# Performance work log

Measured on AMD Instinct MI355X. Metric: run time of the kernel, lower is better.

The kernel has to match this reference:

```python
import jax, jax.numpy as jnp
import numpy as np

NUM_HEADS = 8


def _mha(x, w_in, b_in, w_out, b_out, nh=NUM_HEADS):
    # x: [B, L, H]; torch nn.MultiheadAttention (batch_first) self-attention
    B, L, H = x.shape
    dh = H // nh
    qkv = x @ w_in.T + b_in                      # [B, L, 3H]
    q, k, v = jnp.split(qkv, 3, axis=-1)
    def heads(t):
        return t.reshape(B, L, nh, dh).transpose(0, 2, 1, 3)  # [B, nh, L, dh]
    q, k, v = heads(q), heads(k), heads(v)
    scale = 1.0 / np.sqrt(dh)
    scores = jnp.einsum('bhqd,bhkd->bhqk', q * scale, k)      # [B, nh, L, L]
    attn = jax.nn.softmax(scores, axis=-1)
    out = jnp.einsum('bhqk,bhkd->bhqd', attn, v)               # [B, nh, L, dh]
    out = out.transpose(0, 2, 1, 3).reshape(B, L, H)
    return out @ w_out.T + b_out


def setup_inputs() -> dict:
    key = jax.random.key(0)
    ks = jax.random.split(key, 10)
    S, M, B, H = 64, 4, 128, 1024
    std = 0.02
    inp = {
        'hidden_states_combined': jax.random.normal(ks[0], (S, M, B, 1, H), jnp.float32),
        'mf_in_w': jax.random.normal(ks[1], (3 * H, H), jnp.float32) * std,
        'mf_in_b': jnp.zeros((3 * H,), jnp.float32),
        'mf_out_w': jax.random.normal(ks[2], (H, H), jnp.float32) * std,
        'mf_out_b': jnp.zeros((H,), jnp.float32),
        'sf_in_w': jax.random.normal(ks[3], (3 * H, H), jnp.float32) * std,
        'sf_in_b': jnp.zeros((3 * H,), jnp.float32),
        'sf_out_w': jax.random.normal(ks[4], (H, H), jnp.float32) * std,
        'sf_out_b': jnp.zeros((H,), jnp.float32),
        'pos_enc': jax.random.normal(ks[5], (1, S, H), jnp.float32) * std,
    }
    return inp


def reference(hidden_states_combined, mf_in_w, mf_in_b, mf_out_w, mf_out_b,
              sf_in_w, sf_in_b, sf_out_w, sf_out_b, pos_enc):
    S, M, B, _, H = hidden_states_combined.shape
    # [S, M, B, 1, H] -> [S, B, M, H] -> batch all steps together: [S*B, M, H]
    x = hidden_states_combined[:, :, :, 0, :].transpose(0, 2, 1, 3).reshape(S * B, M, H)
    fused = _mha(x, mf_in_w, mf_in_b, mf_out_w, mf_out_b)        # [S*B, M, H]
    fused = fused.mean(axis=1).reshape(S, B, H)                  # mean over models
    seq = fused.transpose(1, 0, 2) + pos_enc[:, :S, :]            # [B, S, H]
    enhanced = _mha(seq, sf_in_w, sf_in_b, sf_out_w, sf_out_b)   # [B, S, H]
    return enhanced.transpose(1, 0, 2)[:, :, None, :]             # [S, B, 1, H]
```

## Files before the change

kernel.cpp:

```cpp
#include <hip/hip_runtime.h>

typedef unsigned short u16;
typedef __attribute__((ext_vector_type(8))) short bf16x8;
typedef __attribute__((ext_vector_type(4))) float f32x4;

__device__ __forceinline__ u16 f2bf(float f) {
  unsigned u = __float_as_uint(f);
  u += 0x7FFFu + ((u >> 16) & 1u);
  return (u16)(u >> 16);
}
__device__ __forceinline__ float bf2f(u16 h) {
  return __uint_as_float(((unsigned)h) << 16);
}

#define GLOAD16(g, l) __builtin_amdgcn_global_load_lds( \
    (const __attribute__((address_space(1))) void*)(g), \
    (__attribute__((address_space(3))) void*)(l), 16, 0, 0)

__global__ __launch_bounds__(256) void cvtw_kernel(const float* __restrict__ in,
                                                   u16* __restrict__ out, int n4) {
  int i = blockIdx.x * 256 + threadIdx.x;
  if (i >= n4) return;
  float4 f = ((const float4*)in)[i];
  ushort4 u;
  u.x = f2bf(f.x); u.y = f2bf(f.y); u.z = f2bf(f.z); u.w = f2bf(f.w);
  ((ushort4*)out)[i] = u;
}

__global__ __launch_bounds__(256) void xcvt_kernel(const float* __restrict__ hidden,
                                                   u16* __restrict__ xb, int s0) {
  int idx = blockIdx.x * 256 + threadIdx.x;
  int h4 = idx & 255;
  int lrow = idx >> 8;
  int m = lrow & 3;
  int b = (lrow >> 2) & 127;
  int sl = lrow >> 9;
  int s = s0 + sl;
  const float4 f = *(const float4*)(hidden + (((size_t)(s * 4 + m) * 128 + b) * 1024) + h4 * 4);
  ushort4 u;
  u.x = f2bf(f.x); u.y = f2bf(f.y); u.z = f2bf(f.z); u.w = f2bf(f.w);
  *(ushort4*)(xb + (size_t)lrow * 1024 + h4 * 4) = u;
}

template <int KK>
__global__ __launch_bounds__(512, 2) void gemm8p(const u16* __restrict__ A,
                                                 const u16* __restrict__ Bw,
                                                 const float* __restrict__ bias,
                                                 u16* __restrict__ C, int N) {
  __shared__ u16 Sh[65536];
  const int t = threadIdx.x, w = t >> 6, l = t & 63;
  const int lr = l & 15, lg = l >> 4;
  const int wm = w >> 2, wn = w & 3;

  const int gx = gridDim.x;
  const int nb = gx * gridDim.y;
  const int id = blockIdx.y * gx + blockIdx.x;
  const int id2 = (id & 7) * (nb >> 3) + (id >> 3);
  const int rowBase = (id2 / gx) * 256, colBase = (id2 % gx) * 256;

  const int sslot8 = ((t & 3) ^ ((t >> 3) & 3)) * 8;
  const u16* Ag = A + (size_t)(rowBase + (t >> 2)) * KK + sslot8;
  const u16* Bg = Bw + (size_t)(colBase + (t >> 2)) * KK + sslot8;
  const size_t K128 = (size_t)128 * KK;
  const int ldsW = w * 512;

  const int fslot8 = (lg ^ ((lr >> 1) & 3)) * 8;
  const int aRowOff = (wm * 128 + lr) * 32 + fslot8;
  const int bRowOff = (wn * 64 + lr) * 32 + fslot8;

  f32x4 acc[8][4];
#pragma unroll
  for (int i = 0; i < 8; i++)
#pragma unroll
    for (int j = 0; j < 4; j++) acc[i][j] = (f32x4){0.f, 0.f, 0.f, 0.f};
  bf16x8 af[4], bfr[4];

#define STGA(tt, KH, DB) { \
    const u16* g_ = Ag + (size_t)(tt) * 64 + (KH) * 32; \
    GLOAD16(g_, Sh + ((DB) * 2 + (KH)) * 8192 + ldsW); \
    GLOAD16(g_ + K128, Sh + ((DB) * 2 + (KH)) * 8192 + 4096 + ldsW); }
#define STGB(tt, KH, DB) { \
    const u16* g_ = Bg + (size_t)(tt) * 64 + (KH) * 32; \
    GLOAD16(g_, Sh + 32768 + ((DB) * 2 + (KH)) * 8192 + ldsW); \
    GLOAD16(g_ + K128, Sh + 32768 + ((DB) * 2 + (KH)) * 8192 + 4096 + ldsW); }

#define PHASE(DD, KH, MG, DOB, STG, WT) do { \
    const u16* sa_ = Sh + ((DD) * 2 + (KH)) * 8192 + aRowOff; \
    _Pragma("unroll") \
    for (int mi = 0; mi < 4; mi++) af[mi] = *(const bf16x8*)(sa_ + ((MG) * 4 + mi) * 512); \
    if (DOB) { \
      const u16* sb_ = Sh + 32768 + ((DD) * 2 + (KH)) * 8192 + bRowOff; \
      _Pragma("unroll") \
      for (int n = 0; n < 4; n++) bfr[n] = *(const bf16x8*)(sb_ + n * 512); \
    } \
    STG; \
    __builtin_amdgcn_s_barrier(); \
    asm volatile("s_waitcnt lgkmcnt(0)" ::: "memory"); \
    __builtin_amdgcn_sched_barrier(0); \
    __builtin_amdgcn_s_setprio(1); \
    _Pragma("unroll") \
    for (int mi = 0; mi < 4; mi++) { \
      _Pragma("unroll") \
      for (int n = 0; n < 4; n++) \
        acc[(MG) * 4 + mi][n] = \
            __builtin_amdgcn_mfma_f32_16x16x32_bf16(af[mi], bfr[n], acc[(MG) * 4 + mi][n], 0, 0, 0); \
    } \
    __builtin_amdgcn_s_setprio(0); \
    WT; \
    __builtin_amdgcn_s_barrier(); \
  } while (0)

#define WTC(NN) asm volatile("s_waitcnt vmcnt(" #NN ")" ::: "memory")

  STGA(0, 0, 0); STGB(0, 0, 0);
  STGA(0, 1, 0); STGB(0, 1, 0);
  STGA(1, 0, 1); STGB(1, 0, 1);
  WTC(8);
  __builtin_amdgcn_s_barrier();

  const int NIT = KK / 128;
  int t0 = 0;
  for (int it = 0; it < NIT - 1; ++it, t0 += 2) {
    PHASE(0, 0, 0, 1, STGA(t0 + 1, 1, 1), );
    PHASE(0, 0, 1, 0, STGB(t0 + 1, 1, 1), WTC(8));
    PHASE(0, 1, 0, 1, STGA(t0 + 2, 0, 0), );
    PHASE(0, 1, 1, 0, STGB(t0 + 2, 0, 0), WTC(8));
    PHASE(1, 0, 0, 1, STGA(t0 + 2, 1, 0), );
    PHASE(1, 0, 1, 0, STGB(t0 + 2, 1, 0), WTC(8));
    PHASE(1, 1, 0, 1, STGA(t0 + 3, 0, 1), );
    PHASE(1, 1, 1, 0, STGB(t0 + 3, 0, 1), WTC(8));
  }
  PHASE(0, 0, 0, 1, STGA(t0 + 1, 1, 1), );
  PHASE(0, 0, 1, 0, STGB(t0 + 1, 1, 1), WTC(8));
  PHASE(0, 1, 0, 1, , );
  PHASE(0, 1, 1, 0, , WTC(4));
  PHASE(1, 0, 0, 1, , );
  PHASE(1, 0, 1, 0, , WTC(0));
  PHASE(1, 1, 0, 1, , );
  PHASE(1, 1, 1, 0, , );
#undef PHASE
#undef STGA
#undef STGB
#undef WTC

  const int orow0 = rowBase + wm * 128 + lg * 4;
  const int ocol0 = colBase + wn * 64 + lr;
#pragma unroll
  for (int m = 0; m < 8; m++) {
#pragma unroll
    for (int n = 0; n < 4; n++) {
      const int col = ocol0 + n * 16;
      const float bv = bias[col];
#pragma unroll
      for (int r = 0; r < 4; r++) {
        const int row = orow0 + m * 16 + r;
        C[(size_t)row * N + col] = f2bf(acc[m][n][r] + bv);
      }
    }
  }
}

template <int MODE>
__global__ __launch_bounds__(256, 2) void gemm_fp(const u16* __restrict__ A,
                                                  const u16* __restrict__ Bw,
                                                  const float* __restrict__ bias,
                                                  void* __restrict__ Cout,
                                                  int N, int K,
                                                  const float* __restrict__ posenc) {
  __shared__ u16 SA[3][8192];
  __shared__ u16 SB[3][4096];
  const int t = threadIdx.x, w = t >> 6, l = t & 63;
  const int lr = l & 15, lg = l >> 4;
  const int wm = w >> 1, wn = w & 1;

  const int gx = gridDim.x;
  const int nb = gx * gridDim.y;
  const int id = blockIdx.y * gx + blockIdx.x;
  const int id2 = (id & 7) * (nb >> 3) + (id >> 3);
  const int rowBase = (id2 / gx) * 256, colBase = (id2 % gx) * 128;

  const int srow = l >> 2;
  const int ssl = ((l & 3) ^ (srow & 3)) * 8;
  const u16* Ag = A + (size_t)(rowBase + w * 16 + srow) * K + ssl;
  const u16* Bg = Bw + (size_t)(colBase + w * 16 + srow) * K + ssl;
  u16* const lA = &SA[0][0] + w * 512;
  u16* const lB = &SB[0][0] + w * 512;

  const int fsw = (lg ^ (lr & 3)) * 8;
  const int aoff = (wm * 128 + lr) * 32 + fsw;
  const int boff = (wn * 64 + lr) * 32 + fsw;

  f32x4 acc[8][4];
#pragma unroll
  for (int i = 0; i < 8; i++)
#pragma unroll
    for (int j = 0; j < 4; j++) acc[i][j] = (f32x4){0.f, 0.f, 0.f, 0.f};

#define STG_P0(tt, bb) do { \
    const size_t ko_ = (size_t)(tt) * 32; \
    GLOAD16(Ag + ko_,                    lA + (bb) * 8192); \
    GLOAD16(Ag + ko_ + (size_t)64 * K,   lA + (bb) * 8192 + 2048); \
    GLOAD16(Ag + ko_ + (size_t)128 * K,  lA + (bb) * 8192 + 4096); \
  } while (0)
#define STG_P1(tt, bb) do { \
    const size_t ko_ = (size_t)(tt) * 32; \
    GLOAD16(Ag + ko_ + (size_t)192 * K,  lA + (bb) * 8192 + 6144); \
    GLOAD16(Bg + ko_,                    lB + (bb) * 4096); \
    GLOAD16(Bg + ko_ + (size_t)64 * K,   lB + (bb) * 4096 + 2048); \
  } while (0)

  const int nt = K >> 5;
  STG_P0(0, 0); STG_P1(0, 0);
  STG_P0(1, 1); STG_P1(1, 1);
  asm volatile("s_waitcnt vmcnt(6)" ::: "memory");
  __builtin_amdgcn_s_barrier();

  int bcur = 0;
  for (int tt = 0; tt < nt; ++tt) {
    const u16* pa = &SA[bcur][0];
    const u16* pb = &SB[bcur][0];
    const int bnext = (bcur + 2 > 2) ? bcur - 1 : bcur + 2;
    bf16x8 af[4], bfr[4];

#pragma unroll
    for (int m = 0; m < 4; m++) af[m] = *(const bf16x8*)(pa + aoff + m * 512);
#pragma unroll
    for (int n = 0; n < 4; n++) bfr[n] = *(const bf16x8*)(pb + boff + n * 512);
    if (tt + 2 < nt) STG_P0(tt + 2, bnext);
    __builtin_amdgcn_s_barrier();
    asm volatile("s_waitcnt lgkmcnt(0)" ::: "memory");
    __builtin_amdgcn_sched_barrier(0);
    __builtin_amdgcn_s_setprio(1);
#pragma unroll
    for (int m = 0; m < 4; m++)
#pragma unroll
      for (int n = 0; n < 4; n++)
        acc[m][n] = __builtin_amdgcn_mfma_f32_16x16x32_bf16(af[m], bfr[n], acc[m][n], 0, 0, 0);
    __builtin_amdgcn_s_setprio(0);
    __builtin_amdgcn_s_barrier();

#pragma unroll
    for (int m = 0; m < 4; m++) af[m] = *(const bf16x8*)(pa + aoff + (m + 4) * 512);
    if (tt + 2 < nt) STG_P1(tt + 2, bnext);
    __builtin_amdgcn_s_barrier();
    asm volatile("s_waitcnt lgkmcnt(0)" ::: "memory");
    __builtin_amdgcn_sched_barrier(0);
    __builtin_amdgcn_s_setprio(1);
#pragma unroll
    for (int m = 0; m < 4; m++)
#pragma unroll
      for (int n = 0; n < 4; n++)
        acc[m + 4][n] = __builtin_amdgcn_mfma_f32_16x16x32_bf16(af[m], bfr[n], acc[m + 4][n], 0, 0, 0);
    __builtin_amdgcn_s_setprio(0);
    if (tt + 2 < nt) {
      asm volatile("s_waitcnt vmcnt(6)" ::: "memory");
    } else if (tt + 1 < nt) {
      asm volatile("s_waitcnt vmcnt(0)" ::: "memory");
    }
    __builtin_amdgcn_s_barrier();
    bcur = (bcur + 1 > 2) ? 0 : bcur + 1;
  }
#undef STG_P0
#undef STG_P1

  const int orow0 = rowBase + wm * 128 + lg * 4;
  const int ocol0 = colBase + wn * 64 + lr;
#pragma unroll
  for (int m = 0; m < 8; m++) {
#pragma unroll
    for (int n = 0; n < 4; n++) {
      const int col = ocol0 + n * 16;
      const float bv = bias[col];
#pragma unroll
      for (int r = 0; r < 4; r++) {
        const int row = orow0 + m * 16 + r;
        float v = acc[m][n][r] + bv;
        if (MODE == 1) {
          int s = row >> 7, b = row & 127;
          v += posenc[s * 1024 + col];
          ((u16*)Cout)[((size_t)(b * 64 + s)) * 1024 + col] = f2bf(v);
        } else {
          int s = row & 63, b = row >> 6;
          ((float*)Cout)[((size_t)(s * 128 + b)) * 1024 + col] = v;
        }
      }
    }
  }
}

__global__ __launch_bounds__(256) void attn1_kernel(const u16* __restrict__ qkv,
                                                    u16* __restrict__ am, int seqBase) {
  const int w = threadIdx.x >> 6, l = threadIdx.x & 63;
  const int pair = blockIdx.x * 4 + w;
  const int seq = pair >> 3, head = pair & 7;
  const int d0 = l * 2;
  const u16* base = qkv + (size_t)(seq * 4) * 3072 + head * 128 + d0;
  const float scale = 0.08838834764831845f;
  float q[4][2], k[4][2], v[4][2];
#pragma unroll
  for (int m = 0; m < 4; m++) {
    ushort2 uq = *(const ushort2*)(base + (size_t)m * 3072);
    ushort2 uk = *(const ushort2*)(base + (size_t)m * 3072 + 1024);
    ushort2 uv = *(const ushort2*)(base + (size_t)m * 3072 + 2048);
    q[m][0] = bf2f(uq.x) * scale; q[m][1] = bf2f(uq.y) * scale;
    k[m][0] = bf2f(uk.x);         k[m][1] = bf2f(uk.y);
    v[m][0] = bf2f(uv.x);         v[m][1] = bf2f(uv.y);
  }
  float sc[4][4];
#pragma unroll
  for (int i = 0; i < 4; i++)
#pragma unroll
    for (int j = 0; j < 4; j++)
      sc[i][j] = q[i][0] * k[j][0] + q[i][1] * k[j][1];
#pragma unroll
  for (int off = 32; off >= 1; off >>= 1)
#pragma unroll
    for (int i = 0; i < 4; i++)
#pragma unroll
      for (int j = 0; j < 4; j++)
        sc[i][j] += __shfl_xor(sc[i][j], off, 64);
  float pbar[4] = {0.f, 0.f, 0.f, 0.f};
#pragma unroll
  for (int i = 0; i < 4; i++) {
    float mx = fmaxf(fmaxf(sc[i][0], sc[i][1]), fmaxf(sc[i][2], sc[i][3]));
    float e0 = __expf(sc[i][0] - mx), e1 = __expf(sc[i][1] - mx);
    float e2 = __expf(sc[i][2] - mx), e3 = __expf(sc[i][3] - mx);
    float inv = 0.25f / (e0 + e1 + e2 + e3);
    pbar[0] += e0 * inv; pbar[1] += e1 * inv; pbar[2] += e2 * inv; pbar[3] += e3 * inv;
  }
  float o0 = pbar[0] * v[0][0] + pbar[1] * v[1][0] + pbar[2] * v[2][0] + pbar[3] * v[3][0];
  float o1 = pbar[0] * v[0][1] + pbar[1] * v[1][1] + pbar[2] * v[2][1] + pbar[3] * v[3][1];
  ushort2 ou; ou.x = f2bf(o0); ou.y = f2bf(o1);
  *(ushort2*)(am + (size_t)(seqBase + seq) * 1024 + head * 128 + d0) = ou;
}

__global__ __launch_bounds__(256) void attn2_kernel(const u16* __restrict__ qkv2,
                                                    u16* __restrict__ aout) {
  __shared__ u16 Qs[64 * 128];
  __shared__ u16 Ks[64 * 128];
  __shared__ u16 Vt[128 * 72];
  __shared__ u16 Ps[64 * 72];
  const int t = threadIdx.x, w = t >> 6, l = t & 63;
  const int lr = l & 15, lg = l >> 4;
  const int b = blockIdx.x >> 3, head = blockIdx.x & 7;
  const u16* qb = qkv2 + (size_t)(b * 64) * 3072 + head * 128;

#pragma unroll
  for (int c = 0; c < 4; c++) {
    int flat = c * 256 + t;
    int row = flat >> 4, sp = flat & 15;
    int sg = (sp ^ (row & 7)) * 8;
    GLOAD16(qb + (size_t)row * 3072 + sg, Qs + (c * 256 + w * 64) * 8);
    GLOAD16(qb + 1024 + (size_t)row * 3072 + sg, Ks + (c * 256 + w * 64) * 8);
  }
  const int dd = (t & 63) * 2, kb = t >> 6;
#pragma unroll
  for (int c = 0; c < 16; c++) {
    int k = c * 4 + kb;
    ushort2 vv = *(const ushort2*)(qb + 2048 + (size_t)k * 3072 + dd);
    Vt[(size_t)dd * 72 + k] = vv.x;
    Vt[(size_t)(dd + 1) * 72 + k] = vv.y;
  }
  __syncthreads();

  f32x4 sc[4];
#pragma unroll
  for (int cb = 0; cb < 4; cb++) sc[cb] = (f32x4){0.f, 0.f, 0.f, 0.f};
#pragma unroll
  for (int ks = 0; ks < 4; ks++) {
    bf16x8 aq = *(const bf16x8*)(Qs + (w * 16 + lr) * 128 + ((ks * 4 + lg) ^ (lr & 7)) * 8);
#pragma unroll
    for (int cb = 0; cb < 4; cb++) {
      bf16x8 bk = *(const bf16x8*)(Ks + (cb * 16 + lr) * 128 + ((ks * 4 + lg) ^ (lr & 7)) * 8);
      sc[cb] = __builtin_amdgcn_mfma_f32_16x16x32_bf16(aq, bk, sc[cb], 0, 0, 0);
    }
  }

  const float scale = 0.08838834764831845f;
#pragma unroll
  for (int r = 0; r < 4; r++) {
#pragma unroll
    for (int cb = 0; cb < 4; cb++) sc[cb][r] *= scale;
    float mx = fmaxf(fmaxf(sc[0][r], sc[1][r]), fmaxf(sc[2][r], sc[3][r]));
#pragma unroll
    for (int off = 1; off < 16; off <<= 1) mx = fmaxf(mx, __shfl_xor(mx, off, 64));
    float sum = 0.f;
#pragma unroll
    for (int cb = 0; cb < 4; cb++) {
      float e = __expf(sc[cb][r] - mx);
      sum += e;
      sc[cb][r] = e;
    }
#pragma unroll
    for (int off = 1; off < 16; off <<= 1) sum += __shfl_xor(sum, off, 64);
    float inv = 1.f / sum;
    int prow = w * 16 + lg * 4 + r;
#pragma unroll
    for (int cb = 0; cb < 4; cb++)
      Ps[(size_t)prow * 72 + cb * 16 + lr] = f2bf(sc[cb][r] * inv);
  }

  f32x4 o[8];
#pragma unroll
  for (int cb = 0; cb < 8; cb++) o[cb] = (f32x4){0.f, 0.f, 0.f, 0.f};
#pragma unroll
  for (int ks = 0; ks < 2; ks++) {
    bf16x8 ap = *(const bf16x8*)(Ps + (w * 16 + lr) * 72 + ks * 32 + lg * 8);
#pragma unroll
    for (int cb = 0; cb < 8; cb++) {
      bf16x8 bv = *(const bf16x8*)(Vt + (cb * 16 + lr) * 72 + ks * 32 + lg * 8);
      o[cb] = __builtin_amdgcn_mfma_f32_16x16x32_bf16(ap, bv, o[cb], 0, 0, 0);
    }
  }
#pragma unroll
  for (int cb = 0; cb < 8; cb++) {
#pragma unroll
    for (int r = 0; r < 4; r++) {
      int srow = w * 16 + lg * 4 + r;
      int d = cb * 16 + lr;
      aout[(size_t)(b * 64 + srow) * 1024 + head * 128 + d] = f2bf(o[cb][r]);
    }
  }
}

extern "C" void kernel_launch(void* const* d_in, const int* in_sizes, int n_in,
                              void* d_out, int out_size, void* d_ws, size_t ws_size,
                              hipStream_t stream) {
  const float* hidden   = (const float*)d_in[0];
  const float* mf_in_w  = (const float*)d_in[1];
  const float* mf_in_b  = (const float*)d_in[2];
  const float* mf_out_w = (const float*)d_in[3];
  const float* mf_out_b = (const float*)d_in[4];
  const float* sf_in_w  = (const float*)d_in[5];
  const float* sf_in_b  = (const float*)d_in[6];
  const float* sf_out_w = (const float*)d_in[7];
  const float* sf_out_b = (const float*)d_in[8];
  const float* pos_enc  = (const float*)d_in[9];

  char* ws = (char*)d_ws;
  u16* w_mf_in  = (u16*)(ws);
  u16* w_mf_out = (u16*)(ws + 6291456);
  u16* w_sf_in  = (u16*)(ws + 8388608);
  u16* w_sf_out = (u16*)(ws + 14680064);

  cvtw_kernel<<<3072, 256, 0, stream>>>(mf_in_w, w_mf_in, 786432);
  cvtw_kernel<<<1024, 256, 0, stream>>>(mf_out_w, w_mf_out, 262144);
  cvtw_kernel<<<3072, 256, 0, stream>>>(sf_in_w, w_sf_in, 786432);
  cvtw_kernel<<<1024, 256, 0, stream>>>(sf_out_w, w_sf_out, 262144);

  if (ws_size >= 335544320ull) {
    u16* xfull    = (u16*)(ws + 16777216);
    u16* qkvfull  = (u16*)(ws + 83886080);
    u16* attnmean = (u16*)(ws + 285212672);
    u16* seqbuf   = (u16*)(ws + 301989888);
    u16* a2out    = (u16*)(ws + 318767104);

    xcvt_kernel<<<32768, 256, 0, stream>>>(hidden, xfull, 0);
    gemm8p<1024><<<dim3(12, 128), 512, 0, stream>>>(xfull, w_mf_in, mf_in_b, qkvfull, 3072);
    attn1_kernel<<<16384, 256, 0, stream>>>(qkvfull, attnmean, 0);

    gemm_fp<1><<<dim3(8, 32), 256, 0, stream>>>(attnmean, w_mf_out, mf_out_b, seqbuf,
                                                1024, 1024, pos_enc);
    gemm8p<1024><<<dim3(12, 32), 512, 0, stream>>>(seqbuf, w_sf_in, sf_in_b, qkvfull, 3072);
    attn2_kernel<<<1024, 256, 0, stream>>>(qkvfull, a2out);
    gemm_fp<2><<<dim3(8, 32), 256, 0, stream>>>(a2out, w_sf_out, sf_out_b, d_out,
                                                1024, 1024, nullptr);
  } else {
    u16* xchunk   = (u16*)(ws + 16777216);
    u16* qkvbuf   = (u16*)(ws + 33554432);
    u16* attnmean = (u16*)(ws + 83886080);
    u16* seqbuf   = (u16*)(ws + 100663296);
    u16* a2out    = (u16*)(ws + 117440512);

    for (int c = 0; c < 4; ++c) {
      xcvt_kernel<<<8192, 256, 0, stream>>>(hidden, xchunk, c * 16);
      gemm8p<1024><<<dim3(12, 32), 512, 0, stream>>>(xchunk, w_mf_in, mf_in_b, qkvbuf, 3072);
      attn1_kernel<<<4096, 256, 0, stream>>>(qkvbuf, attnmean, c * 2048);
    }

    gemm_fp<1><<<dim3(8, 32), 256, 0, stream>>>(attnmean, w_mf_out, mf_out_b, seqbuf,
                                                1024, 1024, pos_enc);
    gemm8p<1024><<<dim3(12, 32), 512, 0, stream>>>(seqbuf, w_sf_in, sf_in_b, qkvbuf, 3072);
    attn2_kernel<<<1024, 256, 0, stream>>>(qkvbuf, a2out);
    gemm_fp<2><<<dim3(8, 32), 256, 0, stream>>>(a2out, w_sf_out, sf_out_b, d_out,
                                                1024, 1024, nullptr);
  }
}
```

Baseline: 475.4 us.

## Double-buffer GEMM register fragments to overlap LDS reads with MFMA

Restructures the GEMM main loop so the LDS-to-register loads for the next phase are issued before the MFMAs of the current phase, using two register buffers for the A and B fragments. Partial lgkmcnt waits replace the full wait, and one barrier per phase is removed. This is meant to hide LDS read latency behind matrix-core work, at the cost of more VGPRs and trickier waitcnt and barrier correctness.

```diff
diff --git a/kernel.cpp b/kernel.cpp
--- a/kernel.cpp
+++ b/kernel.cpp
@@ -73,7 +73,7 @@
   for (int i = 0; i < 8; i++)
 #pragma unroll
     for (int j = 0; j < 4; j++) acc[i][j] = (f32x4){0.f, 0.f, 0.f, 0.f};
-  bf16x8 af[4], bfr[4];
+  bf16x8 af[2][4], bfr[2][4];
 
 #define STGA(tt, KH, DB) { \
     const u16* g_ = Ag + (size_t)(tt) * 64 + (KH) * 32; \
@@ -84,64 +84,66 @@
     GLOAD16(g_, Sh + 32768 + ((DB) * 2 + (KH)) * 8192 + ldsW); \
     GLOAD16(g_ + K128, Sh + 32768 + ((DB) * 2 + (KH)) * 8192 + 4096 + ldsW); }
 
-#define PHASE(DD, KH, MG, DOB, STG, WT) do { \
+#define RA(DD, KH, MG, BUF) { \
     const u16* sa_ = Sh + ((DD) * 2 + (KH)) * 8192 + aRowOff; \
     _Pragma("unroll") \
-    for (int mi = 0; mi < 4; mi++) af[mi] = *(const bf16x8*)(sa_ + ((MG) * 4 + mi) * 512); \
-    if (DOB) { \
-      const u16* sb_ = Sh + 32768 + ((DD) * 2 + (KH)) * 8192 + bRowOff; \
-      _Pragma("unroll") \
-      for (int n = 0; n < 4; n++) bfr[n] = *(const bf16x8*)(sb_ + n * 512); \
-    } \
-    STG; \
-    __builtin_amdgcn_s_barrier(); \
-    asm volatile("s_waitcnt lgkmcnt(0)" ::: "memory"); \
-    __builtin_amdgcn_sched_barrier(0); \
+    for (int mi = 0; mi < 4; mi++) af[BUF][mi] = *(const bf16x8*)(sa_ + ((MG) * 4 + mi) * 512); }
+#define RB(DD, KH, BUF) { \
+    const u16* sb_ = Sh + 32768 + ((DD) * 2 + (KH)) * 8192 + bRowOff; \
+    _Pragma("unroll") \
+    for (int n = 0; n < 4; n++) bfr[BUF][n] = *(const bf16x8*)(sb_ + n * 512); }
+
+#define LG(NN) asm volatile("s_waitcnt lgkmcnt(" #NN ")" ::: "memory"); \
+               __builtin_amdgcn_sched_barrier(0)
+#define WTC(NN) asm volatile("s_waitcnt vmcnt(" #NN ")" ::: "memory")
+#define BAR __builtin_amdgcn_s_barrier()
+
+#define MM(MG, AB, BB) { \
     __builtin_amdgcn_s_setprio(1); \
     _Pragma("unroll") \
     for (int mi = 0; mi < 4; mi++) { \
       _Pragma("unroll") \
       for (int n = 0; n < 4; n++) \
-        acc[(MG) * 4 + mi][n] = \
-            __builtin_amdgcn_mfma_f32_16x16x32_bf16(af[mi], bfr[n], acc[(MG) * 4 + mi][n], 0, 0, 0); \
+        acc[(MG) * 4 + mi][n] = __builtin_amdgcn_mfma_f32_16x16x32_bf16( \
+            af[AB][mi], bfr[BB][n], acc[(MG) * 4 + mi][n], 0, 0, 0); \
     } \
-    __builtin_amdgcn_s_setprio(0); \
-    WT; \
-    __builtin_amdgcn_s_barrier(); \
-  } while (0)
-
-#define WTC(NN) asm volatile("s_waitcnt vmcnt(" #NN ")" ::: "memory")
+    __builtin_amdgcn_s_setprio(0); }
 
   STGA(0, 0, 0); STGB(0, 0, 0);
   STGA(0, 1, 0); STGB(0, 1, 0);
   STGA(1, 0, 1); STGB(1, 0, 1);
   WTC(8);
-  __builtin_amdgcn_s_barrier();
+  BAR;
+  RA(0, 0, 0, 0); RB(0, 0, 0);
 
   const int NIT = KK / 128;
   int t0 = 0;
   for (int it = 0; it < NIT - 1; ++it, t0 += 2) {
-    PHASE(0, 0, 0, 1, STGA(t0 + 1, 1, 1), );
-    PHASE(0, 0, 1, 0, STGB(t0 + 1, 1, 1), WTC(8));
-    PHASE(0, 1, 0, 1, STGA(t0 + 2, 0, 0), );
-    PHASE(0, 1, 1, 0, STGB(t0 + 2, 0, 0), WTC(8));
-    PHASE(1, 0, 0, 1, STGA(t0 + 2, 1, 0), );
-    PHASE(1, 0, 1, 0, STGB(t0 + 2, 1, 0), WTC(8));
-    PHASE(1, 1, 0, 1, STGA(t0 + 3, 0, 1), );
-    PHASE(1, 1, 1, 0, STGB(t0 + 3, 0, 1), WTC(8));
-  }
-  PHASE(0, 0, 0, 1, STGA(t0 + 1, 1, 1), );
-  PHASE(0, 0, 1, 0, STGB(t0 + 1, 1, 1), WTC(8));
-  PHASE(0, 1, 0, 1, , );
-  PHASE(0, 1, 1, 0, , WTC(4));
-  PHASE(1, 0, 0, 1, , );
-  PHASE(1, 0, 1, 0, , WTC(0));
-  PHASE(1, 1, 0, 1, , );
-  PHASE(1, 1, 1, 0, , );
-#undef PHASE
+    STGA(t0 + 1, 1, 1); RA(0, 0, 1, 1);              LG(4); MM(0, 0, 0); WTC(6); BAR;
+    STGB(t0 + 1, 1, 1); RA(0, 1, 0, 0); RB(0, 1, 1); LG(8); MM(1, 1, 0);         BAR;
+    STGA(t0 + 2, 0, 0); RA(0, 1, 1, 1);              LG(4); MM(0, 0, 1); WTC(6); BAR;
+    STGB(t0 + 2, 0, 0); RA(1, 0, 0, 0); RB(1, 0, 0); LG(8); MM(1, 1, 1);         BAR;
+    STGA(t0 + 2, 1, 0); RA(1, 0, 1, 1);              LG(4); MM(0, 0, 0); WTC(6); BAR;
+    STGB(t0 + 2, 1, 0); RA(1, 1, 0, 0); RB(1, 1, 1); LG(8); MM(1, 1, 0);         BAR;
+    STGA(t0 + 3, 0, 1); RA(1, 1, 1, 1);              LG(4); MM(0, 0, 1); WTC(6); BAR;
+    STGB(t0 + 3, 0, 1); RA(0, 0, 0, 0); RB(0, 0, 0); LG(8); MM(1, 1, 1);         BAR;
+  }
+  STGA(t0 + 1, 1, 1); RA(0, 0, 1, 1);              LG(4); MM(0, 0, 0); WTC(6); BAR;
+  STGB(t0 + 1, 1, 1); RA(0, 1, 0, 0); RB(0, 1, 1); LG(8); MM(1, 1, 0);         BAR;
+  RA(0, 1, 1, 1);                                  LG(4); MM(0, 0, 1); WTC(4); BAR;
+  RA(1, 0, 0, 0); RB(1, 0, 0);                     LG(8); MM(1, 1, 1);         BAR;
+  RA(1, 0, 1, 1);                                  LG(4); MM(0, 0, 0); WTC(0); BAR;
+  RA(1, 1, 0, 0); RB(1, 1, 1);                     LG(8); MM(1, 1, 0);         BAR;
+  RA(1, 1, 1, 1);                                  LG(4); MM(0, 0, 1);         BAR;
+                                                   LG(0); MM(1, 1, 1);
+#undef MM
+#undef BAR
+#undef WTC
+#undef LG
+#undef RB
+#undef RA
+#undef STGB
 #undef STGA
-#undef STGB
-#undef WTC
 
   const int orow0 = rowBase + wm * 128 + lg * 4;
   const int ocol0 = colBase + wn * 64 + lr;
```

After: 471.5 us. No clear change (-0.8%).
